# Kernel tuning notes

Hardware: AMD Instinct MI355X
Metric: run time of the kernel (lower is better)

## Reference

```python
import jax, jax.numpy as jnp
import numpy as np

SCALES = (3, 9, 17, 33)  # must be odd so padding=s//2 preserves spatial size


def _box_conv(img, s):
    # img: [B,1,H,W]; conv with an all-ones s x s kernel, 'same' padding for odd s
    k = jnp.ones((1, 1, s, s), img.dtype)
    p = s // 2
    return jax.lax.conv_general_dilated(
        img, k, window_strides=(1, 1), padding=[(p, p), (p, p)],
        dimension_numbers=("NCHW", "OIHW", "NCHW"))


def setup_inputs() -> dict:
    key = jax.random.key(0)
    B, C, H, W = 8, 3, 1024, 1024
    x = jax.random.normal(key, (B, C, H, W), dtype=jnp.float32)
    # mimicking sparse path-traced samples
    keep = jax.random.uniform(jax.random.fold_in(key, 1), (B, 1, H, W)) >= 0.3
    x = jnp.where(keep, x, 0.0)
    return {"x": x}


def reference(x):
    # F.conv2d(x, ones(1,3,1,1)/3) == per-pixel mean over the 3 channels
    lum = jnp.mean(x, axis=1, keepdims=True)          # [B,1,H,W]
    nonzero = (lum != 0).astype(lum.dtype)            # [B,1,H,W]
    feats = []
    for s in SCALES:
        count = _box_conv(nonzero, s)                 # number of nonzero pixels in window
        pool = _box_conv(lum, s) / jnp.maximum(count, 1.0)  # mean over nonzero pixels
        feats.append(count / float(s * s))            # percentage of nonzero pixels
        feats.append(pool)
    return jnp.concatenate(feats, axis=1)             # [B, 2*len(SCALES), H, W]
```

## Files before the change

kernel.cpp:

```cpp
#include <hip/hip_runtime.h>


constexpr int THREADS = 256;
constexpr int LOADW   = 256;
constexpr int HALO    = 17;
constexpr int COUT    = 223;
constexpr int RING    = 37;
constexpr int ROWSEG  = 32;

__device__ __forceinline__ void barrier_lds() {
    asm volatile("s_waitcnt lgkmcnt(0)" ::: "memory");
    __builtin_amdgcn_s_barrier();
    __builtin_amdgcn_sched_barrier(0);
}

template<int CTRL, int RM>
__device__ __forceinline__ int dppadd_i(int v) {
    int sh = __builtin_amdgcn_update_dpp(0, v, CTRL, RM, 0xF, true);
    return v + sh;
}

__device__ __forceinline__ int wave_iscan_i(int v) {
    v = dppadd_i<0x111, 0xF>(v);
    v = dppadd_i<0x112, 0xF>(v);
    v = dppadd_i<0x114, 0xF>(v);
    v = dppadd_i<0x118, 0xF>(v);
    v = dppadd_i<0x142, 0xA>(v);
    v = dppadd_i<0x143, 0xC>(v);
    return v;
}

__global__ __launch_bounds__(THREADS, 5)
void nzfeat_kernel(const float* __restrict__ x, float* __restrict__ out,
                   int B, int H, int W) {
    constexpr int   PP[4]   = {1, 4, 8, 16};
    constexpr float INVA[4] = {1.f/9.f, 1.f/81.f, 1.f/289.f, 1.f/1089.f};
    constexpr float INVQ    = 1.f / 1024.f;

    __shared__ unsigned short ringL[RING][LOADW];
    __shared__ unsigned char  ringN[RING][LOADW];
    __shared__ int2           wsum[2][2][4];

    const int t    = threadIdx.x;
    const int lane = t & 63;
    const int wv   = t >> 6;

    const int x0 = blockIdx.x * COUT;
    const int y0 = blockIdx.y * ROWSEG;
    const int b  = blockIdx.z;

    const int    gx   = x0 - HALO + t;
    const bool   gxok = (gx >= 0) && (gx < W);
    const int    gxc  = min(max(gx, 0), W - 1);
    const size_t HW   = (size_t)H * W;
    const float* xb   = x + (size_t)b * 3 * HW + gxc;

    auto load_row = [&](int r, float& a0, float& a1, float& a2) {
        const int rc = min(max(r, 0), H - 1);
        const float* p = xb + (size_t)rc * W;
        a0 = p[0]; a1 = p[HW]; a2 = p[2 * HW];
    };

    auto slotOf = [&](int r) { return (int)((unsigned)(r + 2 * RING) % (unsigned)RING); };
    auto wpos   = [&](int v) { return v >= RING ? v - RING : v; };
    auto wneg   = [&](int v) { return v < 0 ? v + RING : v; };

    auto scan_local = [&](float c0, float c1, float c2, int r, int par, int which) -> int2 {
        float lum = 0.f;
        if (gxok && (unsigned)r < (unsigned)H)
            lum = (c0 + c1 + c2) * (1.0f / 3.0f);
        const bool nzb = (lum != 0.f);
        unsigned long long m = __ballot(nzb);
        int below = __builtin_amdgcn_mbcnt_hi((unsigned)(m >> 32),
                      __builtin_amdgcn_mbcnt_lo((unsigned)m, 0));
        int np = below + (nzb ? 1 : 0);
        int q  = (int)rintf(lum * 1024.f);
        int lp = wave_iscan_i(q);
        if (lane == 63) wsum[par][which][wv] = make_int2(lp, np);
        return make_int2(lp, np);
    };

    auto combine_write = [&](int par, int2 A, int2 Bv, int sA, int sB) {
        int oAl = 0, oAn = 0, oBl = 0, oBn = 0;
        #pragma unroll
        for (int w2 = 0; w2 < 3; ++w2)
            if (w2 < wv) {
                int2 u = wsum[par][0][w2]; int2 v = wsum[par][1][w2];
                oAl += u.x; oAn += u.y; oBl += v.x; oBn += v.y;
            }
        ringL[sA][t] = (unsigned short)(A.x + oAl);
        ringN[sA][t] = (unsigned char)(A.y + oAn);
        ringL[sB][t] = (unsigned short)(Bv.x + oBl);
        ringN[sB][t] = (unsigned char)(Bv.y + oBn);
    };

    auto wdiffL = [&](int s, int xlo, int d) -> int {
        int hi = ringL[s][xlo + d], lo = ringL[s][xlo];
        return (int)(short)(unsigned short)(hi - lo);
    };
    auto wdiffN = [&](int s, int xlo, int d) -> int {
        int hi = ringN[s][xlo + d], lo = ringN[s][xlo];
        return (int)(unsigned char)(hi - lo);
    };

    float a0, a1, a2, b0c, b1c, b2c;
    load_row(y0 - 18, a0, a1, a2);
    load_row(y0 - 17, b0c, b1c, b2c);
    for (int i = 0; i < 17; ++i) {
        const int rA = y0 - 18 + 2 * i;
        float n0, n1, n2, m0, m1, m2;
        load_row(rA + 2, n0, n1, n2);
        load_row(rA + 3, m0, m1, m2);
        int2 A  = scan_local(a0, a1, a2, rA, i & 1, 0);
        int2 Bv = scan_local(b0c, b1c, b2c, rA + 1, i & 1, 1);
        barrier_lds();
        combine_write(i & 1, A, Bv, slotOf(rA), slotOf(rA + 1));
        a0 = n0; a1 = n1; a2 = n2; b0c = m0; b1c = m1; b2c = m2;
    }
    barrier_lds();

    const bool activeCol = (t < COUT) && (x0 + t < W);
    float* outb = out + (size_t)b * 8 * HW + (x0 + t);

    int vl[4], vn[4];
    #pragma unroll
    for (int i = 0; i < 4; ++i) {
        const int p  = PP[i];
        const int d  = 2 * p + 1;
        const int x1 = t + HALO - p - 1;
        int sl = 0, sn = 0;
        for (int rr = y0 - 1 - p; rr <= y0 - 1 + p; ++rr) {
            const int s = slotOf(rr);
            sl += wdiffL(s, x1, d);
            sn += wdiffN(s, x1, d);
        }
        vl[i] = sl; vn[i] = sn;
    }

    int sy = slotOf(y0);
    int sw = slotOf(y0 + 16);
    for (int k = 0; k <= ROWSEG / 2; ++k) {
        const bool doScan = (k < ROWSEG / 2);
        int2 A = make_int2(0, 0), Bv = make_int2(0, 0);
        float n0 = 0.f, n1 = 0.f, n2 = 0.f, m0 = 0.f, m1 = 0.f, m2 = 0.f;
        if (doScan) {
            const int wA = y0 + 2 * k + 16;
            if (k < ROWSEG / 2 - 1) {
                load_row(wA + 2, n0, n1, n2);
                load_row(wA + 3, m0, m1, m2);
            }
            A  = scan_local(a0, a1, a2, wA, k & 1, 0);
            Bv = scan_local(b0c, b1c, b2c, wA + 1, k & 1, 1);
        }
        barrier_lds();
        if (doScan) {
            combine_write(k & 1, A, Bv, sw, wpos(sw + 1));
            sw = wpos(sw + 2);
        }
        if (k >= 1) {
            const int ye = y0 + 2 * (k - 1);

            #pragma unroll
            for (int i = 0; i < 4; ++i) {
                const int p  = PP[i];
                const int d  = 2 * p + 1;
                const int x1 = t + HALO - p - 1;
                const int sE = wpos(sy + p);
                const int sL = wneg(sy - 1 - p);
                vl[i] += wdiffL(sE, x1, d) - wdiffL(sL, x1, d);
                vn[i] += wdiffN(sE, x1, d) - wdiffN(sL, x1, d);
            }
            if (activeCol && ye < H) {
                float* o = outb + (size_t)ye * W;
                #pragma unroll
                for (int i = 0; i < 4; ++i) {
                    float cnt = (float)vn[i];
                    o[(size_t)(2 * i) * HW]     = cnt * INVA[i];
                    o[(size_t)(2 * i + 1) * HW] =
                        (float)vl[i] * INVQ * __builtin_amdgcn_rcpf(fmaxf(cnt, 1.f));
                }
            }

            #pragma unroll
            for (int i = 0; i < 4; ++i) {
                const int p  = PP[i];
                const int d  = 2 * p + 1;
                const int x1 = t + HALO - p - 1;
                const int sE = wpos(sy + p + 1);
                const int sL = wneg(sy - p);
                vl[i] += wdiffL(sE, x1, d) - wdiffL(sL, x1, d);
                vn[i] += wdiffN(sE, x1, d) - wdiffN(sL, x1, d);
            }
            if (activeCol && ye + 1 < H) {
                float* o = outb + (size_t)(ye + 1) * W;
                #pragma unroll
                for (int i = 0; i < 4; ++i) {
                    float cnt = (float)vn[i];
                    o[(size_t)(2 * i) * HW]     = cnt * INVA[i];
                    o[(size_t)(2 * i + 1) * HW] =
                        (float)vl[i] * INVQ * __builtin_amdgcn_rcpf(fmaxf(cnt, 1.f));
                }
            }

            sy = wpos(sy + 2);
        }
        a0 = n0; a1 = n1; a2 = n2; b0c = m0; b1c = m1; b2c = m2;
    }
}

extern "C" void kernel_launch(void* const* d_in, const int* in_sizes, int n_in,
                              void* d_out, int out_size, void* d_ws, size_t ws_size,
                              hipStream_t stream) {
    const float* x   = (const float*)d_in[0];
    float*       out = (float*)d_out;

    const int H = 1024, W = 1024;
    const int B = in_sizes[0] / (3 * H * W);

    dim3 grid((W + COUT - 1) / COUT, (H + ROWSEG - 1) / ROWSEG, B);
    nzfeat_kernel<<<grid, dim3(THREADS), 0, stream>>>(x, out, B, H, W);
}
```

Before: 112.3 us.

## Pack row pairs into shared ring words to halve LDS reads

Changes the shared-memory ring so each slot holds two consecutive rows packed into one 32-bit word for the luminance prefix and one 16-bit word for the count prefix. The sliding-window update then reads one packed word per window edge and serves both output rows of a step, instead of issuing separate loads for each row. This cuts the number of LDS load instructions in the inner loop. The cost is extra shift, mask and sign-extension arithmetic and more complex slot indexing for windows that straddle a row pair. Thread columns beyond the output width are also clamped to stay in bounds.

```diff
diff --git a/kernel.cpp b/kernel.cpp
--- a/kernel.cpp
+++ b/kernel.cpp
@@ -5,7 +5,7 @@
 constexpr int LOADW   = 256;
 constexpr int HALO    = 17;
 constexpr int COUT    = 223;
-constexpr int RING    = 37;
+constexpr int RING2   = 19;
 constexpr int ROWSEG  = 32;
 
 __device__ __forceinline__ void barrier_lds() {
@@ -30,6 +30,10 @@
     return v;
 }
 
+__device__ __forceinline__ int sx16(unsigned v) {
+    return (int)(short)(unsigned short)v;
+}
+
 __global__ __launch_bounds__(THREADS, 5)
 void nzfeat_kernel(const float* __restrict__ x, float* __restrict__ out,
                    int B, int H, int W) {
@@ -37,8 +41,8 @@
     constexpr float INVA[4] = {1.f/9.f, 1.f/81.f, 1.f/289.f, 1.f/1089.f};
     constexpr float INVQ    = 1.f / 1024.f;
 
-    __shared__ unsigned short ringL[RING][LOADW];
-    __shared__ unsigned char  ringN[RING][LOADW];
+    __shared__ unsigned int   ringL[RING2][LOADW];
+    __shared__ unsigned short ringN[RING2][LOADW];
     __shared__ int2           wsum[2][2][4];
 
     const int t    = threadIdx.x;
@@ -61,9 +65,9 @@
         a0 = p[0]; a1 = p[HW]; a2 = p[2 * HW];
     };
 
-    auto slotOf = [&](int r) { return (int)((unsigned)(r + 2 * RING) % (unsigned)RING); };
-    auto wpos   = [&](int v) { return v >= RING ? v - RING : v; };
-    auto wneg   = [&](int v) { return v < 0 ? v + RING : v; };
+    auto ps2  = [&](int j) { return (int)((unsigned)(j + 190) % (unsigned)RING2); };
+    auto wpos = [&](int v) { return v >= RING2 ? v - RING2 : v; };
+    auto wneg = [&](int v) { return v < 0 ? v + RING2 : v; };
 
     auto scan_local = [&](float c0, float c1, float c2, int r, int par, int which) -> int2 {
         float lum = 0.f;
@@ -80,7 +84,7 @@
         return make_int2(lp, np);
     };
 
-    auto combine_write = [&](int par, int2 A, int2 Bv, int sA, int sB) {
+    auto combine_write = [&](int par, int2 A, int2 Bv, int pslot) {
         int oAl = 0, oAn = 0, oBl = 0, oBn = 0;
         #pragma unroll
         for (int w2 = 0; w2 < 3; ++w2)
@@ -88,19 +92,39 @@
                 int2 u = wsum[par][0][w2]; int2 v = wsum[par][1][w2];
                 oAl += u.x; oAn += u.y; oBl += v.x; oBn += v.y;
             }
-        ringL[sA][t] = (unsigned short)(A.x + oAl);
-        ringN[sA][t] = (unsigned char)(A.y + oAn);
-        ringL[sB][t] = (unsigned short)(Bv.x + oBl);
-        ringN[sB][t] = (unsigned char)(Bv.y + oBn);
-    };
-
-    auto wdiffL = [&](int s, int xlo, int d) -> int {
-        int hi = ringL[s][xlo + d], lo = ringL[s][xlo];
-        return (int)(short)(unsigned short)(hi - lo);
-    };
-    auto wdiffN = [&](int s, int xlo, int d) -> int {
-        int hi = ringN[s][xlo + d], lo = ringN[s][xlo];
-        return (int)(unsigned char)(hi - lo);
+        unsigned llo = (unsigned)(A.x + oAl) & 0xFFFFu;
+        unsigned lhi = (unsigned)(Bv.x + oBl) & 0xFFFFu;
+        ringL[pslot][t] = (lhi << 16) | llo;
+        unsigned nlo = (unsigned)(A.y + oAn) & 0xFFu;
+        unsigned nhi = (unsigned)(Bv.y + oBn) & 0xFFu;
+        ringN[pslot][t] = (unsigned short)((nhi << 8) | nlo);
+    };
+
+    auto rdAligned = [&](int s, int x1, int d, int& dl0, int& dl1,
+                         int& dn0, int& dn1) {
+        const unsigned int* Lp = &ringL[s][x1];
+        unsigned w0 = Lp[0], w1 = Lp[d];
+        dl0 = sx16(w1 - w0);
+        dl1 = sx16((w1 >> 16) - (w0 >> 16));
+        const unsigned short* Np = &ringN[s][x1];
+        unsigned n0 = Np[0], n1 = Np[d];
+        dn0 = (int)((n1 - n0) & 0xFFu);
+        dn1 = (int)(((n1 >> 8) - (n0 >> 8)) & 0xFFu);
+    };
+    auto rdStraddle = [&](int sH, int sL2, int x1, int d, int& dA, int& dB,
+                          int& nA, int& nB) {
+        const unsigned int* LpH = &ringL[sH][x1];
+        unsigned h0 = LpH[0], h1 = LpH[d];
+        dA = sx16((h1 >> 16) - (h0 >> 16));
+        const unsigned int* LpL = &ringL[sL2][x1];
+        unsigned l0 = LpL[0], l1 = LpL[d];
+        dB = sx16(l1 - l0);
+        const unsigned short* NpH = &ringN[sH][x1];
+        unsigned m0 = NpH[0], m1 = NpH[d];
+        nA = (int)(((m1 >> 8) - (m0 >> 8)) & 0xFFu);
+        const unsigned short* NpL = &ringN[sL2][x1];
+        unsigned k0 = NpL[0], k1 = NpL[d];
+        nB = (int)((k1 - k0) & 0xFFu);
     };
 
     float a0, a1, a2, b0c, b1c, b2c;
@@ -114,12 +138,13 @@
         int2 A  = scan_local(a0, a1, a2, rA, i & 1, 0);
         int2 Bv = scan_local(b0c, b1c, b2c, rA + 1, i & 1, 1);
         barrier_lds();
-        combine_write(i & 1, A, Bv, slotOf(rA), slotOf(rA + 1));
+        combine_write(i & 1, A, Bv, ps2(rA >> 1));
         a0 = n0; a1 = n1; a2 = n2; b0c = m0; b1c = m1; b2c = m2;
     }
     barrier_lds();
 
     const bool activeCol = (t < COUT) && (x0 + t < W);
+    const int  tx = min(t, COUT - 1);
     float* outb = out + (size_t)b * 8 * HW + (x0 + t);
 
     int vl[4], vn[4];
@@ -127,18 +152,27 @@
     for (int i = 0; i < 4; ++i) {
         const int p  = PP[i];
         const int d  = 2 * p + 1;
-        const int x1 = t + HALO - p - 1;
+        const int x1 = tx + HALO - p - 1;
         int sl = 0, sn = 0;
         for (int rr = y0 - 1 - p; rr <= y0 - 1 + p; ++rr) {
-            const int s = slotOf(rr);
-            sl += wdiffL(s, x1, d);
-            sn += wdiffN(s, x1, d);
+            const int s = ps2(rr >> 1);
+            const unsigned int* Lp = &ringL[s][x1];
+            unsigned w0 = Lp[0], w1 = Lp[d];
+            const unsigned short* Np = &ringN[s][x1];
+            unsigned n0 = Np[0], n1 = Np[d];
+            if (rr & 1) {
+                sl += sx16((w1 >> 16) - (w0 >> 16));
+                sn += (int)(((n1 >> 8) - (n0 >> 8)) & 0xFFu);
+            } else {
+                sl += sx16(w1 - w0);
+                sn += (int)((n1 - n0) & 0xFFu);
+            }
         }
         vl[i] = sl; vn[i] = sn;
     }
 
-    int sy = slotOf(y0);
-    int sw = slotOf(y0 + 16);
+    int pc = ps2(y0 >> 1);
+    int pw = ps2((y0 >> 1) + 8);
     for (int k = 0; k <= ROWSEG / 2; ++k) {
         const bool doScan = (k < ROWSEG / 2);
         int2 A = make_int2(0, 0), Bv = make_int2(0, 0);
@@ -154,21 +188,33 @@
         }
         barrier_lds();
         if (doScan) {
-            combine_write(k & 1, A, Bv, sw, wpos(sw + 1));
-            sw = wpos(sw + 2);
+            combine_write(k & 1, A, Bv, pw);
+            pw = wpos(pw + 1);
         }
         if (k >= 1) {
             const int ye = y0 + 2 * (k - 1);
 
+            int eL0[4], eL1[4], eN0[4], eN1[4];
+            int lL0[4], lL1[4], lN0[4], lN1[4];
+            {
+                const int d = 3, x1 = tx + HALO - 2;
+                rdStraddle(pc, wpos(pc + 1), x1, d, eL0[0], eL1[0], eN0[0], eN1[0]);
+                rdAligned (wneg(pc - 1),     x1, d, lL0[0], lL1[0], lN0[0], lN1[0]);
+            }
+            #pragma unroll
+            for (int i = 1; i < 4; ++i) {
+                const int p  = PP[i];
+                const int d  = 2 * p + 1;
+                const int x1 = tx + HALO - p - 1;
+                rdAligned (wpos(pc + p / 2), x1, d, eL0[i], eL1[i], eN0[i], eN1[i]);
+                rdStraddle(wneg(pc - p / 2 - 1), wneg(pc - p / 2), x1, d,
+                           lL0[i], lL1[i], lN0[i], lN1[i]);
+            }
+
             #pragma unroll
             for (int i = 0; i < 4; ++i) {
-                const int p  = PP[i];
-                const int d  = 2 * p + 1;
-                const int x1 = t + HALO - p - 1;
-                const int sE = wpos(sy + p);
-                const int sL = wneg(sy - 1 - p);
-                vl[i] += wdiffL(sE, x1, d) - wdiffL(sL, x1, d);
-                vn[i] += wdiffN(sE, x1, d) - wdiffN(sL, x1, d);
+                vl[i] += eL0[i] - lL0[i];
+                vn[i] += eN0[i] - lN0[i];
             }
             if (activeCol && ye < H) {
                 float* o = outb + (size_t)ye * W;
@@ -183,13 +229,8 @@
 
             #pragma unroll
             for (int i = 0; i < 4; ++i) {
-                const int p  = PP[i];
-                const int d  = 2 * p + 1;
-                const int x1 = t + HALO - p - 1;
-                const int sE = wpos(sy + p + 1);
-                const int sL = wneg(sy - p);
-                vl[i] += wdiffL(sE, x1, d) - wdiffL(sL, x1, d);
-                vn[i] += wdiffN(sE, x1, d) - wdiffN(sL, x1, d);
+                vl[i] += eL1[i] - lL1[i];
+                vn[i] += eN1[i] - lN1[i];
             }
             if (activeCol && ye + 1 < H) {
                 float* o = outb + (size_t)(ye + 1) * W;
@@ -202,7 +243,7 @@
                 }
             }
 
-            sy = wpos(sy + 2);
+            pc = wpos(pc + 1);
         }
         a0 = n0; a1 = n1; a2 = n2; b0c = m0; b1c = m1; b2c = m2;
     }
```

After: 110.5 us. No clear change (-1.5%).
